# Optimization experiments

Measured on AMD Instinct MI355X. Metric: run time of the kernel, lower is better.

Reference implementation:

```python
import jax, jax.numpy as jnp
import numpy as np

NEG_BIG = -9e15  # matches torch's -9000000000000000.0 mask value
LRELU_ALPHA = 0.2


def setup_inputs() -> dict:
    key = jax.random.key(0)
    ks = jax.random.split(key, 6)
    B, N, Fin, Fout = 2, 4096, 64, 64
    x = jax.random.normal(ks[0], (B, N, Fin), jnp.float32)
    pos = jax.random.normal(ks[1], (B, N, 3), jnp.float32)
    # xavier-ish scaled params
    W = jax.random.normal(ks[2], (Fin, Fout), jnp.float32) * (1.0 / np.sqrt(Fin))
    a = jax.random.normal(ks[3], (2 * Fout, 1), jnp.float32) * (1.0 / np.sqrt(2 * Fout))
    Wp = jax.random.normal(ks[4], (3, Fout), jnp.float32) * (1.0 / np.sqrt(3))
    bp = jnp.zeros((Fout,), jnp.float32)
    return {"x": x, "pos": pos, "W": W, "a": a, "Wp": Wp, "bp": bp, "k": 20}


def reference(x, pos, W, a, Wp, bp, k):
    B, N, _ = x.shape
    Fout = W.shape[1]
    Wh = x @ W  # [B,N,Fout]

    # Dynamic kNN graph (adj=None path): squared-distance ranking == cdist ranking
    sq = jnp.sum(pos * pos, axis=-1)  # [B,N]
    d2 = sq[:, :, None] + sq[:, None, :] - 2.0 * jnp.einsum('bnd,bmd->bnm', pos, pos)
    _, idx = jax.lax.top_k(-d2, k + 1)  # smallest k+1 distances
    idx = idx[:, :, 1:]  # drop self
    adj = jnp.zeros((B, N, N), x.dtype).at[
        jnp.arange(B)[:, None, None], jnp.arange(N)[None, :, None], idx
    ].set(1.0)

    # e[b,i,j] = leakyrelu(a1.Wh_i + a2.Wh_j); decompose instead of O(N^2*2F) concat
    f1 = Wh @ a[:Fout]  # [B,N,1]
    f2 = Wh @ a[Fout:]  # [B,N,1]
    e = f1 + jnp.swapaxes(f2, 1, 2)  # [B,N,N]
    e = jnp.where(e > 0, e, LRELU_ALPHA * e)

    e = jnp.where(adj > 0, e, NEG_BIG)
    attn = jax.nn.softmax(e, axis=2)  # dropout is identity in eval mode

    h = jnp.einsum('bnm,bmf->bnf', attn, Wh) + jax.nn.relu(pos @ Wp + bp)
    return jax.nn.elu(h)  # concat=True path
```

## Files before the change

kernel.cpp:

```cpp
#include <hip/hip_runtime.h>
#include <cfloat>

#define NB 4096
#define FD 64
#define QPB 4
#define LRELU_ALPHA 0.2f
#define CCAP 96

__global__ __launch_bounds__(256) void prep_kernel(
    const float* __restrict__ x, const float* __restrict__ pos,
    const float* __restrict__ W, const float* __restrict__ a,
    float* __restrict__ Wh, float* __restrict__ f1, float* __restrict__ f2,
    float4* __restrict__ pq)
{
    const int tid = threadIdx.x;
    if (blockIdx.x >= 512) {
        const int i = (blockIdx.x - 512) * 256 + tid;
        const float px = pos[i * 3 + 0];
        const float py = pos[i * 3 + 1];
        const float pz = pos[i * 3 + 2];
        pq[i] = make_float4(px, py, pz, 0.5f * fmaf(pz, pz, fmaf(py, py, px * px)));
        return;
    }
    __shared__ float sW[FD * FD];
    #pragma unroll
    for (int t = 0; t < 16; ++t) sW[tid + t * 256] = W[tid + t * 256];
    __syncthreads();
    const int lane = tid & 63, wave = tid >> 6;
    const float a1v = a[lane], a2v = a[FD + lane];
    const int rbase = blockIdx.x * 16 + wave * 4;
    #pragma unroll
    for (int j = 0; j < 4; j += 2) {
        const int r0 = rbase + j, r1 = rbase + j + 1;
        const float xv0 = x[((size_t)r0 << 6) + lane];
        const float xv1 = x[((size_t)r1 << 6) + lane];
        float acc0 = 0.f, acc1 = 0.f;
        #pragma unroll
        for (int i = 0; i < FD; ++i) {
            const float wv = sW[i * FD + lane];
            acc0 = fmaf(__shfl(xv0, i, 64), wv, acc0);
            acc1 = fmaf(__shfl(xv1, i, 64), wv, acc1);
        }
        Wh[((size_t)r0 << 6) + lane] = acc0;
        Wh[((size_t)r1 << 6) + lane] = acc1;
        float s10 = acc0 * a1v, s20 = acc0 * a2v;
        float s11 = acc1 * a1v, s21 = acc1 * a2v;
        #pragma unroll
        for (int off = 32; off > 0; off >>= 1) {
            s10 += __shfl_down(s10, off, 64);
            s20 += __shfl_down(s20, off, 64);
            s11 += __shfl_down(s11, off, 64);
            s21 += __shfl_down(s21, off, 64);
        }
        if (lane == 0) { f1[r0] = s10; f2[r0] = s20; f1[r1] = s11; f2[r1] = s21; }
    }
}

__global__ __launch_bounds__(256, 8) void gat_fused(
    const float* __restrict__ pos, const float4* __restrict__ pq,
    const float* __restrict__ Wh,
    const float* __restrict__ f1, const float* __restrict__ f2,
    const float* __restrict__ Wp, const float* __restrict__ bp,
    const int* __restrict__ kptr, float* __restrict__ out)
{
    __shared__ union Pool {
        float tmin[QPB * 256];
        struct {
            unsigned long long pkbuf[QPB][CCAP];
            int cidx[QPB][CCAP];
        } s;
    } pool;
    __shared__ float4 sq[QPB];
    __shared__ float sT[QPB];
    __shared__ unsigned int cnt[QPB];
    __shared__ int idx21[QPB][24];

    const int tid = threadIdx.x;
    const int lane = tid & 63, wave = tid >> 6;
    const int qbase = blockIdx.x * QPB;
    const int b = qbase >> 12;
    const float* posb = pos + (size_t)b * NB * 3;
    const float4* pq4 = pq + ((size_t)b << 12);
    const int k = *kptr;

    if (tid < QPB) {
        const int nq = (qbase + tid) & (NB - 1);
        const float ax = posb[nq * 3 + 0], ay = posb[nq * 3 + 1], az = posb[nq * 3 + 2];
        const float sr = __fadd_rn(__fadd_rn(__fmul_rn(ax, ax), __fmul_rn(ay, ay)),
                                   __fmul_rn(az, az));
        sq[tid] = make_float4(ax, ay, az, sr);
        cnt[tid] = 0;
    }
    if (lane < 24) idx21[wave][lane] = (qbase + wave) & (NB - 1);
    __syncthreads();

    const float4 q0 = sq[0], q1 = sq[1], q2 = sq[2], q3 = sq[3];

    float f0 = FLT_MAX, f1m = FLT_MAX, f2m = FLT_MAX, f3m = FLT_MAX;
    #pragma unroll 4
    for (int t = 0; t < 16; ++t) {
        const float4 p = pq4[t * 256 + tid];
        float d;
        d = p.w - fmaf(q0.x, p.x, fmaf(q0.y, p.y, q0.z * p.z));
        f0 = fminf(f0, d);
        d = p.w - fmaf(q1.x, p.x, fmaf(q1.y, p.y, q1.z * p.z));
        f1m = fminf(f1m, d);
        d = p.w - fmaf(q2.x, p.x, fmaf(q2.y, p.y, q2.z * p.z));
        f2m = fminf(f2m, d);
        d = p.w - fmaf(q3.x, p.x, fmaf(q3.y, p.y, q3.z * p.z));
        f3m = fminf(f3m, d);
    }
    pool.tmin[0 * 256 + tid] = f0;  pool.tmin[1 * 256 + tid] = f1m;
    pool.tmin[2 * 256 + tid] = f2m; pool.tmin[3 * 256 + tid] = f3m;
    __syncthreads();

    float v = fminf(fminf(pool.tmin[wave * 256 + lane],
                          pool.tmin[wave * 256 + 64 + lane]),
                    fminf(pool.tmin[wave * 256 + 128 + lane],
                          pool.tmin[wave * 256 + 192 + lane]));
    #pragma unroll
    for (int kk2 = 2; kk2 <= 64; kk2 <<= 1) {
        #pragma unroll
        for (int j = kk2 >> 1; j > 0; j >>= 1) {
            const float o = __shfl_xor(v, j, 64);
            const bool keepMin = (((lane & j) == 0) == ((lane & kk2) == 0));
            v = keepMin ? fminf(v, o) : fmaxf(v, o);
        }
    }
    const float Tq = __shfl(v, k, 64);
    if (lane == 0) sT[wave] = Tq;
    __syncthreads();

    const float Ts0 = sT[0] + 1e-2f + 1e-3f * fabsf(sT[0]);
    const float Ts1 = sT[1] + 1e-2f + 1e-3f * fabsf(sT[1]);
    const float Ts2 = sT[2] + 1e-2f + 1e-3f * fabsf(sT[2]);
    const float Ts3 = sT[3] + 1e-2f + 1e-3f * fabsf(sT[3]);

    #pragma unroll 4
    for (int t = 0; t < 16; ++t) {
        const int m = t * 256 + tid;
        const float4 p = pq4[m];
        float d;
        d = p.w - fmaf(q0.x, p.x, fmaf(q0.y, p.y, q0.z * p.z));
        if (d <= Ts0) {
            const unsigned int pp = atomicAdd(&cnt[0], 1u);
            if (pp < CCAP) pool.s.cidx[0][pp] = m;
        }
        d = p.w - fmaf(q1.x, p.x, fmaf(q1.y, p.y, q1.z * p.z));
        if (d <= Ts1) {
            const unsigned int pp = atomicAdd(&cnt[1], 1u);
            if (pp < CCAP) pool.s.cidx[1][pp] = m;
        }
        d = p.w - fmaf(q2.x, p.x, fmaf(q2.y, p.y, q2.z * p.z));
        if (d <= Ts2) {
            const unsigned int pp = atomicAdd(&cnt[2], 1u);
            if (pp < CCAP) pool.s.cidx[2][pp] = m;
        }
        d = p.w - fmaf(q3.x, p.x, fmaf(q3.y, p.y, q3.z * p.z));
        if (d <= Ts3) {
            const unsigned int pp = atomicAdd(&cnt[3], 1u);
            if (pp < CCAP) pool.s.cidx[3][pp] = m;
        }
    }
    __syncthreads();

    const float4 qq = sq[wave];
    const int cn0 = (int)cnt[wave];
    const int cn = cn0 < CCAP ? cn0 : CCAP;
    for (int e = lane; e < cn; e += 64) {
        const int m = pool.s.cidx[wave][e];
        const float px = posb[m * 3 + 0];
        const float py = posb[m * 3 + 1];
        const float pz = posb[m * 3 + 2];
        const float sqm = __fadd_rn(__fadd_rn(__fmul_rn(px, px), __fmul_rn(py, py)),
                                    __fmul_rn(pz, pz));
        const float dot = __fadd_rn(__fadd_rn(__fmul_rn(qq.x, px), __fmul_rn(qq.y, py)),
                                    __fmul_rn(qq.z, pz));
        const float d2 = __fsub_rn(__fadd_rn(qq.w, sqm), __fmul_rn(2.0f, dot));
        const unsigned int u = __float_as_uint(d2);
        const unsigned int kk = u ^ ((unsigned int)((int)u >> 31) | 0x80000000u);
        pool.s.pkbuf[wave][e] = ((unsigned long long)kk << 12) | (unsigned int)m;
    }
    for (int e = lane; e < cn; e += 64) {
        const unsigned long long xv = pool.s.pkbuf[wave][e];
        int r = 0;
        for (int j = 0; j < cn; ++j) r += (pool.s.pkbuf[wave][j] < xv);
        if (r <= k) idx21[wave][r] = (int)(xv & 0xFFFu);
    }

    const int row = qbase + wave;
    const bool valid = (lane >= 1 && lane <= k);
    const int nbr = valid ? idx21[wave][lane] : 0;
    const float f1v = f1[row];
    float e = -FLT_MAX;
    if (valid) {
        e = f1v + f2[(b << 12) + nbr];
        e = e > 0.f ? e : LRELU_ALPHA * e;
    }
    float mx = e;
    #pragma unroll
    for (int off = 32; off > 0; off >>= 1) mx = fmaxf(mx, __shfl_xor(mx, off, 64));
    const float ex = valid ? __expf(e - mx) : 0.f;
    float Z = ex;
    #pragma unroll
    for (int off = 32; off > 0; off >>= 1) Z += __shfl_xor(Z, off, 64);
    const float attn = ex / Z;

    const float* whb = Wh + (((size_t)b << 12) << 6);
    float h = 0.f;
    #pragma unroll 4
    for (int t = 1; t <= k; ++t) {
        const int nb_ = __shfl(nbr, t, 64);
        const float s = __shfl(attn, t, 64);
        h = fmaf(s, whb[((size_t)nb_ << 6) + lane], h);
    }

    const float pv = fmaf(qq.x, Wp[0 * FD + lane],
                     fmaf(qq.y, Wp[1 * FD + lane],
                     fmaf(qq.z, Wp[2 * FD + lane], bp[lane])));
    h += pv > 0.f ? pv : 0.f;
    out[((size_t)row << 6) + lane] = h > 0.f ? h : expm1f(h);
}

extern "C" void kernel_launch(void* const* d_in, const int* in_sizes, int n_in,
                              void* d_out, int out_size, void* d_ws, size_t ws_size,
                              hipStream_t stream) {
    const float* x   = (const float*)d_in[0];
    const float* pos = (const float*)d_in[1];
    const float* W   = (const float*)d_in[2];
    const float* a   = (const float*)d_in[3];
    const float* Wp  = (const float*)d_in[4];
    const float* bp  = (const float*)d_in[5];
    const int*   kp  = (const int*)d_in[6];

    float* ws = (float*)d_ws;
    float*  Wh = ws;
    float*  f1 = Wh + 524288;
    float*  f2 = f1 + 8192;
    float4* pq = (float4*)(f2 + 8192);
    float*  out = (float*)d_out;

    prep_kernel<<<544, 256, 0, stream>>>(x, pos, W, a, Wh, f1, f2, pq);
    gat_fused<<<(NB * 2) / QPB, 256, 0, stream>>>(pos, pq, Wh, f1, f2, Wp, bp, kp, out);
}
```

Baseline: 101.9 us.

## Process eight queries per block with two queries per wave in kNN attention

Doubles the number of queries handled per block from 4 to 8. Each streamed point tile is now scored against eight queries instead of four, and each wave handles the threshold, candidate ranking and attention for two queries in sequence. Query coordinates are loaded into wave-uniform scalar registers with readfirstlane. This halves how often the position array is re-streamed overall, at the cost of more registers, fewer blocks and serialized per-wave tail work.

```diff
diff --git a/kernel.cpp b/kernel.cpp
--- a/kernel.cpp
+++ b/kernel.cpp
@@ -3,9 +3,13 @@
 
 #define NB 4096
 #define FD 64
-#define QPB 4
+#define QPB 8
 #define LRELU_ALPHA 0.2f
 #define CCAP 96
+
+__device__ __forceinline__ float rfl(float v) {
+    return __int_as_float(__builtin_amdgcn_readfirstlane(__float_as_int(v)));
+}
 
 __global__ __launch_bounds__(256) void prep_kernel(
     const float* __restrict__ x, const float* __restrict__ pos,
@@ -91,135 +95,138 @@
         sq[tid] = make_float4(ax, ay, az, sr);
         cnt[tid] = 0;
     }
-    if (lane < 24) idx21[wave][lane] = (qbase + wave) & (NB - 1);
-    __syncthreads();
-
-    const float4 q0 = sq[0], q1 = sq[1], q2 = sq[2], q3 = sq[3];
-
-    float f0 = FLT_MAX, f1m = FLT_MAX, f2m = FLT_MAX, f3m = FLT_MAX;
+    if (lane < 24) {
+        idx21[2 * wave][lane]     = (qbase + 2 * wave) & (NB - 1);
+        idx21[2 * wave + 1][lane] = (qbase + 2 * wave + 1) & (NB - 1);
+    }
+    __syncthreads();
+
+    float qx[QPB], qy[QPB], qz[QPB];
+    #pragma unroll
+    for (int i = 0; i < QPB; ++i) {
+        const int nq = (qbase + i) & (NB - 1);
+        qx[i] = rfl(posb[nq * 3 + 0]);
+        qy[i] = rfl(posb[nq * 3 + 1]);
+        qz[i] = rfl(posb[nq * 3 + 2]);
+    }
+
+    float mn[QPB];
+    #pragma unroll
+    for (int i = 0; i < QPB; ++i) mn[i] = FLT_MAX;
     #pragma unroll 4
     for (int t = 0; t < 16; ++t) {
         const float4 p = pq4[t * 256 + tid];
-        float d;
-        d = p.w - fmaf(q0.x, p.x, fmaf(q0.y, p.y, q0.z * p.z));
-        f0 = fminf(f0, d);
-        d = p.w - fmaf(q1.x, p.x, fmaf(q1.y, p.y, q1.z * p.z));
-        f1m = fminf(f1m, d);
-        d = p.w - fmaf(q2.x, p.x, fmaf(q2.y, p.y, q2.z * p.z));
-        f2m = fminf(f2m, d);
-        d = p.w - fmaf(q3.x, p.x, fmaf(q3.y, p.y, q3.z * p.z));
-        f3m = fminf(f3m, d);
-    }
-    pool.tmin[0 * 256 + tid] = f0;  pool.tmin[1 * 256 + tid] = f1m;
-    pool.tmin[2 * 256 + tid] = f2m; pool.tmin[3 * 256 + tid] = f3m;
-    __syncthreads();
-
-    float v = fminf(fminf(pool.tmin[wave * 256 + lane],
-                          pool.tmin[wave * 256 + 64 + lane]),
-                    fminf(pool.tmin[wave * 256 + 128 + lane],
-                          pool.tmin[wave * 256 + 192 + lane]));
-    #pragma unroll
-    for (int kk2 = 2; kk2 <= 64; kk2 <<= 1) {
-        #pragma unroll
-        for (int j = kk2 >> 1; j > 0; j >>= 1) {
-            const float o = __shfl_xor(v, j, 64);
-            const bool keepMin = (((lane & j) == 0) == ((lane & kk2) == 0));
-            v = keepMin ? fminf(v, o) : fmaxf(v, o);
-        }
-    }
-    const float Tq = __shfl(v, k, 64);
-    if (lane == 0) sT[wave] = Tq;
-    __syncthreads();
-
-    const float Ts0 = sT[0] + 1e-2f + 1e-3f * fabsf(sT[0]);
-    const float Ts1 = sT[1] + 1e-2f + 1e-3f * fabsf(sT[1]);
-    const float Ts2 = sT[2] + 1e-2f + 1e-3f * fabsf(sT[2]);
-    const float Ts3 = sT[3] + 1e-2f + 1e-3f * fabsf(sT[3]);
-
-    #pragma unroll 4
+        #pragma unroll
+        for (int i = 0; i < QPB; ++i) {
+            const float d = p.w - fmaf(qx[i], p.x, fmaf(qy[i], p.y, qz[i] * p.z));
+            mn[i] = fminf(mn[i], d);
+        }
+    }
+    #pragma unroll
+    for (int i = 0; i < QPB; ++i) pool.tmin[i * 256 + tid] = mn[i];
+    __syncthreads();
+
+    #pragma unroll
+    for (int qi = 0; qi < 2; ++qi) {
+        const int q = 2 * wave + qi;
+        float v = fminf(fminf(pool.tmin[q * 256 + lane],
+                              pool.tmin[q * 256 + 64 + lane]),
+                        fminf(pool.tmin[q * 256 + 128 + lane],
+                              pool.tmin[q * 256 + 192 + lane]));
+        #pragma unroll
+        for (int kk2 = 2; kk2 <= 64; kk2 <<= 1) {
+            #pragma unroll
+            for (int j = kk2 >> 1; j > 0; j >>= 1) {
+                const float o = __shfl_xor(v, j, 64);
+                const bool keepMin = (((lane & j) == 0) == ((lane & kk2) == 0));
+                v = keepMin ? fminf(v, o) : fmaxf(v, o);
+            }
+        }
+        const float Tq = __shfl(v, k, 64);
+        if (lane == 0) sT[q] = Tq;
+    }
+    __syncthreads();
+
+    float Ts[QPB];
+    #pragma unroll
+    for (int i = 0; i < QPB; ++i)
+        Ts[i] = sT[i] + 1e-2f + 1e-3f * fabsf(sT[i]);
+
+    #pragma unroll 2
     for (int t = 0; t < 16; ++t) {
         const int m = t * 256 + tid;
         const float4 p = pq4[m];
-        float d;
-        d = p.w - fmaf(q0.x, p.x, fmaf(q0.y, p.y, q0.z * p.z));
-        if (d <= Ts0) {
-            const unsigned int pp = atomicAdd(&cnt[0], 1u);
-            if (pp < CCAP) pool.s.cidx[0][pp] = m;
-        }
-        d = p.w - fmaf(q1.x, p.x, fmaf(q1.y, p.y, q1.z * p.z));
-        if (d <= Ts1) {
-            const unsigned int pp = atomicAdd(&cnt[1], 1u);
-            if (pp < CCAP) pool.s.cidx[1][pp] = m;
-        }
-        d = p.w - fmaf(q2.x, p.x, fmaf(q2.y, p.y, q2.z * p.z));
-        if (d <= Ts2) {
-            const unsigned int pp = atomicAdd(&cnt[2], 1u);
-            if (pp < CCAP) pool.s.cidx[2][pp] = m;
-        }
-        d = p.w - fmaf(q3.x, p.x, fmaf(q3.y, p.y, q3.z * p.z));
-        if (d <= Ts3) {
-            const unsigned int pp = atomicAdd(&cnt[3], 1u);
-            if (pp < CCAP) pool.s.cidx[3][pp] = m;
-        }
-    }
-    __syncthreads();
-
-    const float4 qq = sq[wave];
-    const int cn0 = (int)cnt[wave];
-    const int cn = cn0 < CCAP ? cn0 : CCAP;
-    for (int e = lane; e < cn; e += 64) {
-        const int m = pool.s.cidx[wave][e];
-        const float px = posb[m * 3 + 0];
-        const float py = posb[m * 3 + 1];
-        const float pz = posb[m * 3 + 2];
-        const float sqm = __fadd_rn(__fadd_rn(__fmul_rn(px, px), __fmul_rn(py, py)),
-                                    __fmul_rn(pz, pz));
-        const float dot = __fadd_rn(__fadd_rn(__fmul_rn(qq.x, px), __fmul_rn(qq.y, py)),
-                                    __fmul_rn(qq.z, pz));
-        const float d2 = __fsub_rn(__fadd_rn(qq.w, sqm), __fmul_rn(2.0f, dot));
-        const unsigned int u = __float_as_uint(d2);
-        const unsigned int kk = u ^ ((unsigned int)((int)u >> 31) | 0x80000000u);
-        pool.s.pkbuf[wave][e] = ((unsigned long long)kk << 12) | (unsigned int)m;
-    }
-    for (int e = lane; e < cn; e += 64) {
-        const unsigned long long xv = pool.s.pkbuf[wave][e];
-        int r = 0;
-        for (int j = 0; j < cn; ++j) r += (pool.s.pkbuf[wave][j] < xv);
-        if (r <= k) idx21[wave][r] = (int)(xv & 0xFFFu);
-    }
-
-    const int row = qbase + wave;
-    const bool valid = (lane >= 1 && lane <= k);
-    const int nbr = valid ? idx21[wave][lane] : 0;
-    const float f1v = f1[row];
-    float e = -FLT_MAX;
-    if (valid) {
-        e = f1v + f2[(b << 12) + nbr];
-        e = e > 0.f ? e : LRELU_ALPHA * e;
-    }
-    float mx = e;
-    #pragma unroll
-    for (int off = 32; off > 0; off >>= 1) mx = fmaxf(mx, __shfl_xor(mx, off, 64));
-    const float ex = valid ? __expf(e - mx) : 0.f;
-    float Z = ex;
-    #pragma unroll
-    for (int off = 32; off > 0; off >>= 1) Z += __shfl_xor(Z, off, 64);
-    const float attn = ex / Z;
-
-    const float* whb = Wh + (((size_t)b << 12) << 6);
-    float h = 0.f;
-    #pragma unroll 4
-    for (int t = 1; t <= k; ++t) {
-        const int nb_ = __shfl(nbr, t, 64);
-        const float s = __shfl(attn, t, 64);
-        h = fmaf(s, whb[((size_t)nb_ << 6) + lane], h);
-    }
-
-    const float pv = fmaf(qq.x, Wp[0 * FD + lane],
-                     fmaf(qq.y, Wp[1 * FD + lane],
-                     fmaf(qq.z, Wp[2 * FD + lane], bp[lane])));
-    h += pv > 0.f ? pv : 0.f;
-    out[((size_t)row << 6) + lane] = h > 0.f ? h : expm1f(h);
+        #pragma unroll
+        for (int i = 0; i < QPB; ++i) {
+            const float d = p.w - fmaf(qx[i], p.x, fmaf(qy[i], p.y, qz[i] * p.z));
+            if (d <= Ts[i]) {
+                const unsigned int pp = atomicAdd(&cnt[i], 1u);
+                if (pp < CCAP) pool.s.cidx[i][pp] = m;
+            }
+        }
+    }
+    __syncthreads();
+
+    #pragma unroll
+    for (int qi = 0; qi < 2; ++qi) {
+        const int q = 2 * wave + qi;
+        const float4 qq = sq[q];
+        const int cn0 = (int)cnt[q];
+        const int cn = cn0 < CCAP ? cn0 : CCAP;
+        for (int e = lane; e < cn; e += 64) {
+            const int m = pool.s.cidx[q][e];
+            const float px = posb[m * 3 + 0];
+            const float py = posb[m * 3 + 1];
+            const float pz = posb[m * 3 + 2];
+            const float sqm = __fadd_rn(__fadd_rn(__fmul_rn(px, px), __fmul_rn(py, py)),
+                                        __fmul_rn(pz, pz));
+            const float dot = __fadd_rn(__fadd_rn(__fmul_rn(qq.x, px), __fmul_rn(qq.y, py)),
+                                        __fmul_rn(qq.z, pz));
+            const float d2 = __fsub_rn(__fadd_rn(qq.w, sqm), __fmul_rn(2.0f, dot));
+            const unsigned int u = __float_as_uint(d2);
+            const unsigned int kk = u ^ ((unsigned int)((int)u >> 31) | 0x80000000u);
+            pool.s.pkbuf[q][e] = ((unsigned long long)kk << 12) | (unsigned int)m;
+        }
+        for (int e = lane; e < cn; e += 64) {
+            const unsigned long long xv = pool.s.pkbuf[q][e];
+            int r = 0;
+            for (int j = 0; j < cn; ++j) r += (pool.s.pkbuf[q][j] < xv);
+            if (r <= k) idx21[q][r] = (int)(xv & 0xFFFu);
+        }
+
+        const int row = qbase + q;
+        const bool valid = (lane >= 1 && lane <= k);
+        const int nbr = valid ? idx21[q][lane] : 0;
+        const float f1v = f1[row];
+        float e = -FLT_MAX;
+        if (valid) {
+            e = f1v + f2[(b << 12) + nbr];
+            e = e > 0.f ? e : LRELU_ALPHA * e;
+        }
+        float mx = e;
+        #pragma unroll
+        for (int off = 32; off > 0; off >>= 1) mx = fmaxf(mx, __shfl_xor(mx, off, 64));
+        const float ex = valid ? __expf(e - mx) : 0.f;
+        float Z = ex;
+        #pragma unroll
+        for (int off = 32; off > 0; off >>= 1) Z += __shfl_xor(Z, off, 64);
+        const float attn = ex / Z;
+
+        const float* whb = Wh + (((size_t)b << 12) << 6);
+        float h = 0.f;
+        #pragma unroll 4
+        for (int t = 1; t <= k; ++t) {
+            const int nb_ = __shfl(nbr, t, 64);
+            const float s = __shfl(attn, t, 64);
+            h = fmaf(s, whb[((size_t)nb_ << 6) + lane], h);
+        }
+
+        const float pv = fmaf(qq.x, Wp[0 * FD + lane],
+                         fmaf(qq.y, Wp[1 * FD + lane],
+                         fmaf(qq.z, Wp[2 * FD + lane], bp[lane])));
+        h += pv > 0.f ? pv : 0.f;
+        out[((size_t)row << 6) + lane] = h > 0.f ? h : expm1f(h);
+    }
 }
 
 extern "C" void kernel_launch(void* const* d_in, const int* in_sizes, int n_in,
```

New measurement: 110.0 us. 8.0% more time.
